# Optimization experiments

Measured on AMD Instinct MI355X. Metric: run time of the kernel, lower is better.

Reference implementation:

```python
import jax, jax.numpy as jnp
import numpy as np

B, T, D = 4096, 200, 64
H1, H2 = 64, 32


def _prelu(x, a):
    # PReLU with a single learnable slope (torch default num_parameters=1)
    return jnp.where(x >= 0, x, a * x)


def setup_inputs() -> dict:
    key = jax.random.key(0)
    ks = jax.random.split(key, 10)
    behavior = jax.random.normal(ks[0], (B, T, D), dtype=jnp.float32)
    candidate = jax.random.normal(ks[1], (B, D), dtype=jnp.float32)
    mask = jax.random.randint(ks[2], (B, T), 0, 2) > 0
    in_dim = 4 * D
    W1 = jax.random.normal(ks[3], (in_dim, H1), dtype=jnp.float32) / np.sqrt(in_dim)
    b1 = jnp.zeros((H1,), dtype=jnp.float32)
    a1 = jnp.full((1,), 0.25, dtype=jnp.float32)  # torch PReLU default init
    W2 = jax.random.normal(ks[4], (H1, H2), dtype=jnp.float32) / np.sqrt(H1)
    b2 = jnp.zeros((H2,), dtype=jnp.float32)
    a2 = jnp.full((1,), 0.25, dtype=jnp.float32)
    W3 = jax.random.normal(ks[5], (H2, 1), dtype=jnp.float32) / np.sqrt(H2)
    b3 = jnp.zeros((1,), dtype=jnp.float32)
    return {"behavior": behavior, "candidate": candidate, "mask": mask,
            "W1": W1, "b1": b1, "a1": a1,
            "W2": W2, "b2": b2, "a2": a2,
            "W3": W3, "b3": b3}


def reference(behavior, candidate, mask, W1, b1, a1, W2, b2, a2, W3, b3):
    # behavior: [B,T,D], candidate: [B,D], mask: [B,T] bool
    cand = candidate[:, None, :]                       # [B,1,D]
    cand_exp = jnp.broadcast_to(cand, behavior.shape)  # [B,T,D]
    diff = behavior - cand_exp
    prod = behavior * cand_exp
    att_input = jnp.concatenate([behavior, cand_exp, diff, prod], axis=-1)  # [B,T,4D]
    h = _prelu(att_input @ W1 + b1, a1)
    h = _prelu(h @ W2 + b2, a2)
    logits = (h @ W3 + b3)[..., 0]                     # [B,T]
    logits = jnp.where(mask, logits, -jnp.inf)
    w = jax.nn.softmax(logits, axis=-1)                # [B,T]
    user_interest = jnp.einsum('bt,btd->bd', w, behavior)  # [B,D]
    return user_interest
```

## Files before the change

kernel.cpp:

```cpp
#include <hip/hip_runtime.h>
#include <hip/hip_bf16.h>

#define T_LEN   200
#define NTILES  13

typedef __bf16 bf16x8 __attribute__((ext_vector_type(8)));
typedef __bf16 bf16x4 __attribute__((ext_vector_type(4)));
typedef float  f32x4  __attribute__((ext_vector_type(4)));

#if __has_builtin(__builtin_amdgcn_mfma_f32_16x16x16_bf16)
#define MFMA16(a, b, c) __builtin_amdgcn_mfma_f32_16x16x16_bf16((a), (b), (c), 0, 0, 0)
#elif __has_builtin(__builtin_amdgcn_mfma_f32_16x16x16bf16_1k)
#define MFMA16(a, b, c) __builtin_amdgcn_mfma_f32_16x16x16bf16_1k((a), (b), (c), 0, 0, 0)
#else
static __device__ __forceinline__ f32x4 mfma16_asm(bf16x4 a, bf16x4 b, f32x4 c) {
  asm("v_mfma_f32_16x16x16_bf16 %0, %1, %2, %0" : "+v"(c) : "v"(a), "v"(b));
  return c;
}
#define MFMA16(a, b, c) mfma16_asm((a), (b), (c))
#endif

#define MFMA32(a, b, c) __builtin_amdgcn_mfma_f32_16x16x32_bf16((a), (b), (c), 0, 0, 0)

struct __align__(16) Smem {
  unsigned char w1ac[64 * 144];
  unsigned char w1d [64 * 144];
  float biasL[4][64];
};

__device__ __forceinline__ void loadA(const float* __restrict__ behB, int t, int kb,
                                      f32x4 (&x)[4]) {
  if (t < T_LEN) {
    const float* p = behB + (size_t)t * 64 + kb;
    x[0] = *(const f32x4*)p;
    x[1] = *(const f32x4*)(p + 4);
    x[2] = *(const f32x4*)(p + 32);
    x[3] = *(const f32x4*)(p + 36);
  } else {
    x[0] = f32x4{0.f, 0.f, 0.f, 0.f};
    x[1] = f32x4{0.f, 0.f, 0.f, 0.f};
    x[2] = f32x4{0.f, 0.f, 0.f, 0.f};
    x[3] = f32x4{0.f, 0.f, 0.f, 0.f};
  }
}

__global__ __launch_bounds__(256, 3) void lau_kernel(
    const float* __restrict__ behG, const float* __restrict__ candG,
    const int*  __restrict__ maskG,
    const float* __restrict__ W1g, const float* __restrict__ b1g, const float* __restrict__ a1g,
    const float* __restrict__ W2g, const float* __restrict__ b2g, const float* __restrict__ a2g,
    const float* __restrict__ W3g,
    float* __restrict__ outG)
{
  __shared__ Smem s;
  const int tid  = threadIdx.x;
  const int lane = tid & 63;
  const int wv   = tid >> 6;
  const int b    = blockIdx.x * 4 + wv;
  const int r    = lane & 15;
  const int g    = lane >> 4;
  const int kb   = g * 8;

  const float* candB = candG + (size_t)b * 64;

  for (int idx = tid; idx < 4096; idx += 256) {
    int j = idx & 63, d = idx >> 6;
    float ac = W1g[d * 64 + j] + W1g[(128 + d) * 64 + j];
    float dd = W1g[(192 + d) * 64 + j];
    *(__bf16*)(s.w1ac + j * 144 + d * 2) = (__bf16)ac;
    *(__bf16*)(s.w1d  + j * 144 + d * 2) = (__bf16)dd;
  }
  {
    float biasv = b1g[lane];
#pragma unroll 8
    for (int d = 0; d < 64; ++d) {
      float wd = W1g[(64 + d) * 64 + lane] - W1g[(128 + d) * 64 + lane];
      biasv += candB[d] * wd;
    }
    s.biasL[wv][lane] = biasv;
  }
  __syncthreads();

  const bool boolmask = (__ballot(((const unsigned int*)maskG)[lane] > 1u) != 0ull);

  const f32x4 c0a = *(const f32x4*)(candB + kb);
  const f32x4 c0b = *(const f32x4*)(candB + kb + 4);
  const f32x4 c1a = *(const f32x4*)(candB + kb + 32);
  const f32x4 c1b = *(const f32x4*)(candB + kb + 36);

  bf16x8 A1[4][2];
#pragma unroll
  for (int f = 0; f < 8; ++f) {
    const int jt = f >> 1, kc = f & 1;
    const int rowoff = (jt * 16 + r) * 144 + kc * 64 + g * 16;
    bf16x8 ac = *(const bf16x8*)(s.w1ac + rowoff);
    bf16x8 dd = *(const bf16x8*)(s.w1d  + rowoff);
    f32x4 cA = kc ? c1a : c0a;
    f32x4 cB = kc ? c1b : c0b;
    bf16x8 o;
#pragma unroll
    for (int e = 0; e < 4; ++e) {
      o[e]     = (__bf16)((float)ac[e]     + cA[e] * (float)dd[e]);
      o[4 + e] = (__bf16)((float)ac[4 + e] + cB[e] * (float)dd[4 + e]);
    }
    A1[jt][kc] = o;
  }

  bf16x4 W2f[8];
#pragma unroll
  for (int f = 0; f < 8; ++f) {
    const int nt = f >> 2, c = f & 3;
#pragma unroll
    for (int i = 0; i < 4; ++i)
      W2f[f][i] = (__bf16)W2g[(c * 16 + g * 4 + i) * 32 + nt * 16 + r];
  }

  f32x4 bj4[4];
#pragma unroll
  for (int jt = 0; jt < 4; ++jt)
#pragma unroll
    for (int i = 0; i < 4; ++i)
      bj4[jt][i] = s.biasL[wv][jt * 16 + g * 4 + i];

  const float al1 = a1g[0];
  const float al2 = a2g[0];
  const f32x4 cinit0 = *(const f32x4*)(b2g + g * 4);
  const f32x4 cinit1 = *(const f32x4*)(b2g + 16 + g * 4);
  const f32x4 w3f0   = *(const f32x4*)(W3g + g * 4);
  const f32x4 w3f1   = *(const f32x4*)(W3g + 16 + g * 4);

  const float* behB = behG + (size_t)b * T_LEN * 64;
  const unsigned char* maskB8 = (const unsigned char*)maskG + (size_t)b * T_LEN;
  const int* maskB32 = maskG + (size_t)b * T_LEN;

  float mrun = -__builtin_inff();
  float srun = 0.f;
  f32x4 o0 = {0,0,0,0}, o1 = {0,0,0,0}, o2 = {0,0,0,0}, o3 = {0,0,0,0};

  f32x4 xc[4];
  loadA(behB, r, kb, xc);
  int mc = boolmask ? (int)maskB8[r] : maskB32[r];

#pragma unroll 1
  for (int mt = 0; mt < NTILES; ++mt) {
    bf16x8 ab0, ab1;
#pragma unroll
    for (int i = 0; i < 4; ++i) {
      ab0[i]     = (__bf16)xc[0][i];
      ab0[4 + i] = (__bf16)xc[1][i];
      ab1[i]     = (__bf16)xc[2][i];
      ab1[4 + i] = (__bf16)xc[3][i];
    }
    const int mcur = mc;
    if (mt + 1 < NTILES) {
      int tn = (mt + 1) * 16 + r;
      loadA(behB, tn, kb, xc);
      mc = (tn < T_LEN) ? (boolmask ? (int)maskB8[tn] : maskB32[tn]) : 0;
    }

    bf16x4 a2f[4];
#pragma unroll
    for (int jt = 0; jt < 4; ++jt) {
      f32x4 acc = MFMA32(A1[jt][0], ab0, bj4[jt]);
      acc = MFMA32(A1[jt][1], ab1, acc);
#pragma unroll
      for (int i = 0; i < 4; ++i) {
        float h = acc[i];
        h = (h >= 0.f) ? h : al1 * h;
        a2f[jt][i] = (__bf16)h;
      }
    }

    f32x4 acc20 = cinit0, acc21 = cinit1;
#pragma unroll
    for (int c = 0; c < 4; ++c) acc20 = MFMA16(W2f[c],     a2f[c], acc20);
#pragma unroll
    for (int c = 0; c < 4; ++c) acc21 = MFMA16(W2f[4 + c], a2f[c], acc21);

    float partial = 0.f;
#pragma unroll
    for (int i = 0; i < 4; ++i) {
      float h0 = acc20[i]; h0 = (h0 >= 0.f) ? h0 : al2 * h0;
      float h1 = acc21[i]; h1 = (h1 >= 0.f) ? h1 : al2 * h1;
      partial += h0 * w3f0[i] + h1 * w3f1[i];
    }
    partial += __shfl_xor(partial, 16);
    partial += __shfl_xor(partial, 32);

    const bool valid = ((mt * 16 + r) < T_LEN) && (mcur != 0);
    float lvt = valid ? partial : -__builtin_inff();
    if (lvt > mrun + 8.f) {
      float fs = __expf(mrun - lvt);
      srun *= fs;
#pragma unroll
      for (int i = 0; i < 4; ++i) { o0[i] *= fs; o1[i] *= fs; o2[i] *= fs; o3[i] *= fs; }
      mrun = lvt;
    }
    float et = valid ? __expf(lvt - mrun) : 0.f;
    srun += et;
#pragma unroll
    for (int i = 0; i < 4; ++i) {
      o0[i] += et * (float)ab0[i];
      o1[i] += et * (float)ab0[4 + i];
      o2[i] += et * (float)ab1[i];
      o3[i] += et * (float)ab1[4 + i];
    }
  }

  float M = mrun;
#pragma unroll
  for (int off = 1; off < 16; off <<= 1) M = fmaxf(M, __shfl_xor(M, off));
  {
    float fac = __expf(mrun - M);
    srun *= fac;
#pragma unroll
    for (int i = 0; i < 4; ++i) { o0[i] *= fac; o1[i] *= fac; o2[i] *= fac; o3[i] *= fac; }
  }
#pragma unroll
  for (int off = 1; off < 16; off <<= 1) {
#pragma unroll
    for (int i = 0; i < 4; ++i) {
      o0[i] += __shfl_xor(o0[i], off);
      o1[i] += __shfl_xor(o1[i], off);
      o2[i] += __shfl_xor(o2[i], off);
      o3[i] += __shfl_xor(o3[i], off);
    }
    srun += __shfl_xor(srun, off);
  }
  if (r == 0) {
    float inv = 1.f / srun;
    float* po = outG + (size_t)b * 64 + kb;
#pragma unroll
    for (int i = 0; i < 4; ++i) {
      o0[i] *= inv; o1[i] *= inv; o2[i] *= inv; o3[i] *= inv;
    }
    *(f32x4*)(po)      = o0;
    *(f32x4*)(po + 4)  = o1;
    *(f32x4*)(po + 32) = o2;
    *(f32x4*)(po + 36) = o3;
  }
}

extern "C" void kernel_launch(void* const* d_in, const int* in_sizes, int n_in,
                              void* d_out, int out_size, void* d_ws, size_t ws_size,
                              hipStream_t stream) {
  (void)n_in; (void)d_ws; (void)ws_size; (void)out_size;
  const float* beh  = (const float*)d_in[0];
  const float* cand = (const float*)d_in[1];
  const int*   mask = (const int*)d_in[2];
  const float* W1   = (const float*)d_in[3];
  const float* b1   = (const float*)d_in[4];
  const float* a1   = (const float*)d_in[5];
  const float* W2   = (const float*)d_in[6];
  const float* b2   = (const float*)d_in[7];
  const float* a2   = (const float*)d_in[8];
  const float* W3   = (const float*)d_in[9];

  int B = in_sizes[1] / 64;
  int grid = B / 4;
  lau_kernel<<<grid, 256, 0, stream>>>(beh, cand, mask, W1, b1, a1, W2, b2, a2, W3,
                                       (float*)d_out);
}
```

Measured before the change: 58.61 us.

## Prefetch behavior tiles two ahead and preload mask into a bitmask

Double-buffers the behavior tile loads so each tile is fetched two iterations ahead, with the loop manually unrolled by two across two register buffers. The per-tile mask loads are replaced by a single upfront gather into a per-lane bitmask, which takes those loads out of the main loop's dependency chain. The aim is to hide global memory latency better. In exchange it uses more registers under launch_bounds(256,3), which may cause spills or lower occupancy.

```diff
diff --git a/kernel.cpp b/kernel.cpp
--- a/kernel.cpp
+++ b/kernel.cpp
@@ -83,6 +83,17 @@
 
   const bool boolmask = (__ballot(((const unsigned int*)maskG)[lane] > 1u) != 0ull);
 
+  const unsigned char* maskB8 = (const unsigned char*)maskG + (size_t)b * T_LEN;
+  const int* maskB32 = maskG + (size_t)b * T_LEN;
+  unsigned mbits = 0;
+#pragma unroll
+  for (int mt = 0; mt < NTILES; ++mt) {
+    int t = mt * 16 + r;
+    int mv = 0;
+    if (t < T_LEN) mv = boolmask ? (int)maskB8[t] : maskB32[t];
+    mbits |= (mv != 0 ? 1u : 0u) << mt;
+  }
+
   const f32x4 c0a = *(const f32x4*)(candB + kb);
   const f32x4 c0b = *(const f32x4*)(candB + kb + 4);
   const f32x4 c1a = *(const f32x4*)(candB + kb + 32);
@@ -130,82 +141,81 @@
   const f32x4 w3f1   = *(const f32x4*)(W3g + 16 + g * 4);
 
   const float* behB = behG + (size_t)b * T_LEN * 64;
-  const unsigned char* maskB8 = (const unsigned char*)maskG + (size_t)b * T_LEN;
-  const int* maskB32 = maskG + (size_t)b * T_LEN;
 
   float mrun = -__builtin_inff();
   float srun = 0.f;
   f32x4 o0 = {0,0,0,0}, o1 = {0,0,0,0}, o2 = {0,0,0,0}, o3 = {0,0,0,0};
 
-  f32x4 xc[4];
-  loadA(behB, r, kb, xc);
-  int mc = boolmask ? (int)maskB8[r] : maskB32[r];
+  f32x4 xa[4], xb[4];
+  loadA(behB, r, kb, xa);
+  loadA(behB, 16 + r, kb, xb);
+
+#define BODY(XC, MT, PFT, DOPF) do {                                          \
+    bf16x8 ab0, ab1;                                                          \
+    _Pragma("unroll")                                                         \
+    for (int i = 0; i < 4; ++i) {                                             \
+      ab0[i]     = (__bf16)XC[0][i];                                          \
+      ab0[4 + i] = (__bf16)XC[1][i];                                          \
+      ab1[i]     = (__bf16)XC[2][i];                                          \
+      ab1[4 + i] = (__bf16)XC[3][i];                                          \
+    }                                                                         \
+    if (DOPF) loadA(behB, (PFT) * 16 + r, kb, XC);                            \
+    bf16x4 a2f[4];                                                            \
+    _Pragma("unroll")                                                         \
+    for (int jt = 0; jt < 4; ++jt) {                                          \
+      f32x4 acc = MFMA32(A1[jt][0], ab0, bj4[jt]);                            \
+      acc = MFMA32(A1[jt][1], ab1, acc);                                      \
+      _Pragma("unroll")                                                       \
+      for (int i = 0; i < 4; ++i) {                                           \
+        float h = acc[i];                                                     \
+        h = (h >= 0.f) ? h : al1 * h;                                         \
+        a2f[jt][i] = (__bf16)h;                                               \
+      }                                                                       \
+    }                                                                         \
+    f32x4 acc20 = cinit0, acc21 = cinit1;                                     \
+    _Pragma("unroll")                                                         \
+    for (int c = 0; c < 4; ++c) acc20 = MFMA16(W2f[c],     a2f[c], acc20);    \
+    _Pragma("unroll")                                                         \
+    for (int c = 0; c < 4; ++c) acc21 = MFMA16(W2f[4 + c], a2f[c], acc21);    \
+    float partial = 0.f;                                                      \
+    _Pragma("unroll")                                                         \
+    for (int i = 0; i < 4; ++i) {                                             \
+      float h0 = acc20[i]; h0 = (h0 >= 0.f) ? h0 : al2 * h0;                  \
+      float h1 = acc21[i]; h1 = (h1 >= 0.f) ? h1 : al2 * h1;                  \
+      partial += h0 * w3f0[i] + h1 * w3f1[i];                                 \
+    }                                                                         \
+    partial += __shfl_xor(partial, 16);                                       \
+    partial += __shfl_xor(partial, 32);                                       \
+    const bool valid = ((mbits >> (MT)) & 1u) != 0u;                          \
+    float lvt = valid ? partial : -__builtin_inff();                          \
+    if (lvt > mrun + 8.f) {                                                   \
+      float fs = __expf(mrun - lvt);                                          \
+      srun *= fs;                                                             \
+      _Pragma("unroll")                                                       \
+      for (int i = 0; i < 4; ++i) {                                           \
+        o0[i] *= fs; o1[i] *= fs; o2[i] *= fs; o3[i] *= fs;                   \
+      }                                                                       \
+      mrun = lvt;                                                             \
+    }                                                                         \
+    float et = valid ? __expf(lvt - mrun) : 0.f;                              \
+    srun += et;                                                               \
+    _Pragma("unroll")                                                         \
+    for (int i = 0; i < 4; ++i) {                                             \
+      o0[i] += et * (float)ab0[i];                                            \
+      o1[i] += et * (float)ab0[4 + i];                                        \
+      o2[i] += et * (float)ab1[i];                                            \
+      o3[i] += et * (float)ab1[4 + i];                                        \
+    }                                                                         \
+  } while (0)
 
 #pragma unroll 1
-  for (int mt = 0; mt < NTILES; ++mt) {
-    bf16x8 ab0, ab1;
-#pragma unroll
-    for (int i = 0; i < 4; ++i) {
-      ab0[i]     = (__bf16)xc[0][i];
-      ab0[4 + i] = (__bf16)xc[1][i];
-      ab1[i]     = (__bf16)xc[2][i];
-      ab1[4 + i] = (__bf16)xc[3][i];
-    }
-    const int mcur = mc;
-    if (mt + 1 < NTILES) {
-      int tn = (mt + 1) * 16 + r;
-      loadA(behB, tn, kb, xc);
-      mc = (tn < T_LEN) ? (boolmask ? (int)maskB8[tn] : maskB32[tn]) : 0;
-    }
-
-    bf16x4 a2f[4];
-#pragma unroll
-    for (int jt = 0; jt < 4; ++jt) {
-      f32x4 acc = MFMA32(A1[jt][0], ab0, bj4[jt]);
-      acc = MFMA32(A1[jt][1], ab1, acc);
-#pragma unroll
-      for (int i = 0; i < 4; ++i) {
-        float h = acc[i];
-        h = (h >= 0.f) ? h : al1 * h;
-        a2f[jt][i] = (__bf16)h;
-      }
-    }
-
-    f32x4 acc20 = cinit0, acc21 = cinit1;
-#pragma unroll
-    for (int c = 0; c < 4; ++c) acc20 = MFMA16(W2f[c],     a2f[c], acc20);
-#pragma unroll
-    for (int c = 0; c < 4; ++c) acc21 = MFMA16(W2f[4 + c], a2f[c], acc21);
-
-    float partial = 0.f;
-#pragma unroll
-    for (int i = 0; i < 4; ++i) {
-      float h0 = acc20[i]; h0 = (h0 >= 0.f) ? h0 : al2 * h0;
-      float h1 = acc21[i]; h1 = (h1 >= 0.f) ? h1 : al2 * h1;
-      partial += h0 * w3f0[i] + h1 * w3f1[i];
-    }
-    partial += __shfl_xor(partial, 16);
-    partial += __shfl_xor(partial, 32);
-
-    const bool valid = ((mt * 16 + r) < T_LEN) && (mcur != 0);
-    float lvt = valid ? partial : -__builtin_inff();
-    if (lvt > mrun + 8.f) {
-      float fs = __expf(mrun - lvt);
-      srun *= fs;
-#pragma unroll
-      for (int i = 0; i < 4; ++i) { o0[i] *= fs; o1[i] *= fs; o2[i] *= fs; o3[i] *= fs; }
-      mrun = lvt;
-    }
-    float et = valid ? __expf(lvt - mrun) : 0.f;
-    srun += et;
-#pragma unroll
-    for (int i = 0; i < 4; ++i) {
-      o0[i] += et * (float)ab0[i];
-      o1[i] += et * (float)ab0[4 + i];
-      o2[i] += et * (float)ab1[i];
-      o3[i] += et * (float)ab1[4 + i];
-    }
-  }
+  for (int mt = 0; mt < NTILES - 1; mt += 2) {
+    BODY(xa, mt,     mt + 2, true);
+    BODY(xb, mt + 1, mt + 3, (mt + 3) < NTILES);
+  }
+  BODY(xa, NTILES - 1, 0, false);
+
+#undef BODY
 
   float M = mrun;
 #pragma unroll
```

New measurement: 73.29 us. +25.0%, slower.
